# Optimization experiments

Hardware: AMD Instinct MI355X
Metric: run time of the kernel (lower is better)

## Reference

```python
import jax, jax.numpy as jnp
import numpy as np

# dims
N, E, B, T = 1024, 8192, 4, 8          # nodes, edges, batch, time steps
IN, HID, H, NCLASS = 64, 64, 4, 7      # in_dim, nhidden, heads, nclass
K = N - NCLASS + 1                     # output-head conv width
NEG, EPS = 0.2, 1e-5


def setup_inputs() -> dict:
    key = jax.random.key(0)
    ks = jax.random.split(key, 24)
    p = lambda i, shape: jax.random.normal(ks[i], shape, jnp.float32) * 0.05
    inputs = jax.random.normal(ks[0], (B, IN, T, N), jnp.float32)
    src = jax.random.randint(ks[1], (E,), 0, N, jnp.int32)
    dst = jnp.repeat(jnp.arange(N, dtype=jnp.int32), E // N)  # every node has in-degree 8
    return {
        "inputs": inputs, "src": src, "dst": dst,
        "W0": p(2, (H * HID, IN)), "al0": p(3, (H, HID)), "ar0": p(4, (H, HID)),
        "W1": p(5, (H * HID, H * HID)), "al1": p(6, (H, HID)), "ar1": p(7, (H, HID)),
        "W2": p(8, (H * 1, H * HID)), "al2": p(9, (H, 1)), "ar2": p(10, (H, 1)),
        "Wres2": p(11, (H * 1, H * HID)),
        # Outputlayer
        "tc1_w": p(12, (H, H, T)), "tc1_b": p(13, (H,)),
        "ln1_g": jnp.ones((N, H), jnp.float32), "ln1_b": jnp.zeros((N, H), jnp.float32),
        "tc2_w": p(14, (1, H)), "tc2_b": p(15, (1,)),
        "ln2_g": jnp.ones((N, 1), jnp.float32), "ln2_b": jnp.zeros((N, 1), jnp.float32),
        "fc_w": p(16, (K,)), "fc_b": p(17, (1,)),
    }


def _gat_conv(h, src, dst, W, al, ar, res=None, act=None):
    # h: (N,B,T,F) -> feat: (N,B,T,H,D)
    heads, d = al.shape
    feat = (h @ W.T).reshape(N, B, T, heads, d)
    el = jnp.einsum('nbthd,hd->nbth', feat, al)
    er = jnp.einsum('nbthd,hd->nbth', feat, ar)
    e = jax.nn.leaky_relu(el[src] + er[dst], NEG)           # (E,B,T,H)
    emax = jax.ops.segment_max(e, dst, num_segments=N)
    ex = jnp.exp(e - emax[dst])
    den = jax.ops.segment_sum(ex, dst, num_segments=N)
    a = ex / den[dst]                                        # edge softmax over incoming edges
    out = jax.ops.segment_sum(feat[src] * a[..., None], dst, num_segments=N)  # (N,B,T,H,D)
    if res is not None:
        out = out + res
    if act is not None:
        out = act(out)
    return out


def reference(inputs, src, dst,
              W0, al0, ar0, W1, al1, ar1, W2, al2, ar2, Wres2,
              tc1_w, tc1_b, ln1_g, ln1_b, tc2_w, tc2_b, ln2_g, ln2_b, fc_w, fc_b):
    # (B,IN,T,N) -> (N,B,T,IN) : transpose(0,3).transpose(1,3)
    h = jnp.transpose(inputs.astype(jnp.float32), (3, 0, 2, 1))
    h1 = _gat_conv(h, src, dst, W0, al0, ar0, act=jax.nn.elu).reshape(N, B, T, H * HID)
    h2 = _gat_conv(h1, src, dst, W1, al1, ar1,
                   res=h1.reshape(N, B, T, H, HID), act=jax.nn.elu).reshape(N, B, T, H * HID)
    res2 = (h2 @ Wres2.T).reshape(N, B, T, H, 1)
    o = _gat_conv(h2, src, dst, W2, al2, ar2, res=res2)      # (N,B,T,H,1)
    # transpose(1,3).transpose(0,3).squeeze(-1) -> (B,H,T,N)
    x = jnp.transpose(o[..., 0], (1, 3, 2, 0))

    # Outputlayer
    # tconv1: Conv2d(H->H, kernel (T,1)) collapses time -> (B,H,N)
    x1 = jnp.einsum('oht,bhtn->bon', tc1_w, x) + tc1_b[None, :, None]
    # ln1: LayerNorm over (N,H) of (B,1,N,H)
    z = jnp.transpose(x1, (0, 2, 1))                          # (B,N,H)
    mu = z.mean(axis=(1, 2), keepdims=True)
    var = z.var(axis=(1, 2), keepdims=True)
    z = (z - mu) / jnp.sqrt(var + EPS) * ln1_g + ln1_b
    x1 = jnp.transpose(z, (0, 2, 1))                          # (B,H,N)
    # tconv2: 1x1 conv H->1 -> (B,1,N)
    x2 = jnp.einsum('oh,bhn->bon', tc2_w, x1) + tc2_b[None, :, None]
    # ln2: LayerNorm over (N,1)
    mu = x2.mean(axis=2, keepdims=True)
    var = x2.var(axis=2, keepdims=True)
    x2 = (x2 - mu) / jnp.sqrt(var + EPS) * ln2_g[:, 0] + ln2_b[:, 0]
    # fc: Conv2d(1->1, kernel (1,K)) sliding over nodes -> (B,NCLASS)
    xc = x2[:, :, None, :]                                    # (B,1,1,N) NCHW
    w = fc_w[None, None, None, :]                             # (1,1,1,K) OIHW
    out = jax.lax.conv_general_dilated(xc, w, (1, 1), 'VALID') + fc_b[None, :, None, None]
    return out[:, 0, 0, :]                                    # (B, NCLASS)
```

## Files before the change

### kernel.cpp

```cpp
#include <hip/hip_runtime.h>
#include <math.h>

#define NEGS 0.2f
#define EPSF 1e-5f

typedef short s16x8 __attribute__((ext_vector_type(8)));
typedef float f32x4 __attribute__((ext_vector_type(4)));

__device__ __forceinline__ float b2f(unsigned short u) {
  union { unsigned int i; float f; } v; v.i = ((unsigned int)u) << 16; return v.f;
}
__device__ __forceinline__ unsigned short f2b(float f) {
  union { float f; unsigned int i; } v; v.f = f;
  unsigned int x = v.i;
  return (unsigned short)((x + 0x7fffu + ((x >> 16) & 1u)) >> 16);
}

__device__ __forceinline__ float block_reduce256(float v, float* red) {
  #pragma unroll
  for (int o = 32; o > 0; o >>= 1) v += __shfl_down(v, o);
  __syncthreads();
  if ((threadIdx.x & 63) == 0) red[threadIdx.x >> 6] = v;
  __syncthreads();
  return red[0] + red[1] + red[2] + red[3];
}

__global__ __launch_bounds__(256) void k_cvt(
    const float* __restrict__ inp, const float* __restrict__ W0,
    const float* __restrict__ W1, unsigned short* __restrict__ Xb,
    unsigned short* __restrict__ W0b, unsigned short* __restrict__ W1b)
{
  __shared__ float L[64][65];
  const int tid = threadIdx.x;
  if (blockIdx.x >= 512) {
    const int j = (blockIdx.x - 512) * 256 + tid;
    W0b[j] = f2b(W0[j]);
    float4 w4 = *(const float4*)&W1[j*4];
    ushort4 o4; o4.x = f2b(w4.x); o4.y = f2b(w4.y); o4.z = f2b(w4.z); o4.w = f2b(w4.w);
    *(ushort4*)&W1b[j*4] = o4;
    return;
  }
  const int blk = blockIdx.x;
  const int n0 = (blk & 15) * 64;
  const int t  = (blk >> 4) & 7;
  const int b  = blk >> 7;
  const int nn = tid & 63, ch0 = tid >> 6;
  #pragma unroll
  for (int ch = ch0; ch < 64; ch += 4)
    L[ch][nn] = inp[((size_t)(b*64 + ch)*8 + t)*1024 + n0 + nn];
  __syncthreads();
  const int r = tid >> 2, ck = tid & 3;
  s16x8 o0, o1;
  #pragma unroll
  for (int i = 0; i < 8; ++i) o0[i] = (short)f2b(L[ck*16 + i][r]);
  #pragma unroll
  for (int i = 0; i < 8; ++i) o1[i] = (short)f2b(L[ck*16 + 8 + i][r]);
  const int row = (n0 + r)*32 + b*8 + t;
  *(s16x8*)&Xb[(size_t)row*64 + ck*16]     = o0;
  *(s16x8*)&Xb[(size_t)row*64 + ck*16 + 8] = o1;
}

template<int KD>
__global__ __launch_bounds__(256) void k_feat_mfma(
    const unsigned short* __restrict__ X, const unsigned short* __restrict__ Wb,
    const float* __restrict__ al, const float* __restrict__ ar,
    unsigned short* __restrict__ feat, float* __restrict__ el, float* __restrict__ er)
{
  __shared__ __align__(16) unsigned short Lb[64*256];
  const int tid  = threadIdx.x;
  const int w    = tid >> 6;
  const int lane = tid & 63;
  const int n16  = lane & 15;
  const int q    = lane >> 4;
  const int r0   = blockIdx.x * 64;

  f32x4 acc[4][4];
  #pragma unroll
  for (int rt = 0; rt < 4; ++rt)
    #pragma unroll
    for (int ct = 0; ct < 4; ++ct) acc[rt][ct] = (f32x4){0.f,0.f,0.f,0.f};

  #pragma unroll
  for (int kc = 0; kc < KD/32; ++kc) {
    s16x8 af[4], bf[4];
    #pragma unroll
    for (int rt = 0; rt < 4; ++rt)
      af[rt] = *(const s16x8*)&X[(size_t)(r0 + rt*16 + n16)*KD + kc*32 + q*8];
    #pragma unroll
    for (int ct = 0; ct < 4; ++ct)
      bf[ct] = *(const s16x8*)&Wb[(size_t)((w*4 + ct)*16 + n16)*KD + kc*32 + q*8];
    #pragma unroll
    for (int rt = 0; rt < 4; ++rt)
      #pragma unroll
      for (int ct = 0; ct < 4; ++ct)
        acc[rt][ct] = __builtin_amdgcn_mfma_f32_16x16x32_bf16(af[rt], bf[ct], acc[rt][ct], 0, 0, 0);
  }

  float alv[4], arv[4];
  #pragma unroll
  for (int ct = 0; ct < 4; ++ct) {
    alv[ct] = al[w*64 + ct*16 + n16];
    arv[ct] = ar[w*64 + ct*16 + n16];
  }
  #pragma unroll
  for (int rt = 0; rt < 4; ++rt) {
    #pragma unroll
    for (int reg = 0; reg < 4; ++reg) {
      float pl = acc[rt][0][reg]*alv[0] + acc[rt][1][reg]*alv[1]
               + acc[rt][2][reg]*alv[2] + acc[rt][3][reg]*alv[3];
      float pr = acc[rt][0][reg]*arv[0] + acc[rt][1][reg]*arv[1]
               + acc[rt][2][reg]*arv[2] + acc[rt][3][reg]*arv[3];
      #pragma unroll
      for (int o = 1; o < 16; o <<= 1) { pl += __shfl_xor(pl, o); pr += __shfl_xor(pr, o); }
      if (n16 == 0) {
        int r = r0 + rt*16 + q*4 + reg;
        el[r*4 + w] = pl;
        er[r*4 + w] = pr;
      }
    }
  }

  #pragma unroll
  for (int rt = 0; rt < 4; ++rt)
    #pragma unroll
    for (int ct = 0; ct < 4; ++ct)
      #pragma unroll
      for (int reg = 0; reg < 4; ++reg)
        Lb[(rt*16 + q*4 + reg)*256 + w*64 + ct*16 + n16] = f2b(acc[rt][ct][reg]);
  __syncthreads();
  #pragma unroll
  for (int i = 0; i < 8; ++i) {
    int u = tid + i*256;
    int row = u >> 5, off = (u & 31) * 8;
    *(s16x8*)&feat[(size_t)(r0 + row)*256 + off] = *(const s16x8*)&Lb[row*256 + off];
  }
}

template<int RES, int STOREOUT, int PROJ>
__global__ __launch_bounds__(256) void k_agg(
    const unsigned short* __restrict__ feat, const float* __restrict__ el,
    const float* __restrict__ er, const int* __restrict__ src,
    const unsigned short* __restrict__ resin, unsigned short* __restrict__ out,
    const float* __restrict__ W2, const float* __restrict__ Wres2,
    float* __restrict__ feat2, float* __restrict__ res2)
{
  __shared__ float wsm[8][4][8][4];
  __shared__ int   ssm[8];
  __shared__ __align__(16) float Wp[8][256];
  const int n   = blockIdx.x;
  const int tid = threadIdx.x;
  if (tid < 8) ssm[tid] = src[n*8 + tid];
  if (PROJ) {
    for (int j = tid; j < 2048; j += 256) {
      int o = j >> 8, k = j & 255;
      Wp[o][k] = (o < 4) ? W2[o*256 + k] : Wres2[(o-4)*256 + k];
    }
  }
  __syncthreads();
  if (tid < 128) {
    const int h = tid & 3, t = (tid >> 2) & 7, b = tid >> 5;
    const int rn = n*32 + b*8 + t;
    const float erv = er[rn*4 + h];
    float e[8]; float m = -1e30f;
    #pragma unroll
    for (int j = 0; j < 8; ++j) {
      float v = el[(ssm[j]*32 + b*8 + t)*4 + h] + erv;
      v = v >= 0.f ? v : NEGS * v;
      e[j] = v; m = fmaxf(m, v);
    }
    float den = 0.f;
    #pragma unroll
    for (int j = 0; j < 8; ++j) { e[j] = __expf(e[j] - m); den += e[j]; }
    const float inv = 1.f / den;
    #pragma unroll
    for (int j = 0; j < 8; ++j) wsm[j][b][t][h] = e[j] * inv;
  }
  __syncthreads();
  const int b    = tid >> 6;
  const int lane = tid & 63;
  const int c0   = lane * 4;
  const int h    = lane >> 4;
  int s[8];
  #pragma unroll
  for (int j = 0; j < 8; ++j) s[j] = ssm[j];
  #pragma unroll 1
  for (int t = 0; t < 8; ++t) {
    const int rn = n*32 + b*8 + t;
    float a0=0.f, a1=0.f, a2=0.f, a3=0.f;
    #pragma unroll
    for (int j = 0; j < 8; ++j) {
      ushort4 u = *(const ushort4*)&feat[(size_t)(s[j]*32 + b*8 + t)*256 + c0];
      const float wj = wsm[j][b][t][h];
      a0 = fmaf(wj, b2f(u.x), a0); a1 = fmaf(wj, b2f(u.y), a1);
      a2 = fmaf(wj, b2f(u.z), a2); a3 = fmaf(wj, b2f(u.w), a3);
    }
    if (RES) {
      ushort4 rr = *(const ushort4*)&resin[(size_t)rn*256 + c0];
      a0 += b2f(rr.x); a1 += b2f(rr.y); a2 += b2f(rr.z); a3 += b2f(rr.w);
      a0 = a0 > 0.f ? a0 : expm1f(a0);
      a1 = a1 > 0.f ? a1 : expm1f(a1);
      a2 = a2 > 0.f ? a2 : expm1f(a2);
      a3 = a3 > 0.f ? a3 : expm1f(a3);
    } else {
      a0 = a0 > 0.f ? a0 : expm1f(a0);
      a1 = a1 > 0.f ? a1 : expm1f(a1);
      a2 = a2 > 0.f ? a2 : expm1f(a2);
      a3 = a3 > 0.f ? a3 : expm1f(a3);
    }
    if (STOREOUT) {
      ushort4 o;
      o.x = f2b(a0); o.y = f2b(a1); o.z = f2b(a2); o.w = f2b(a3);
      *(ushort4*)&out[(size_t)rn*256 + c0] = o;
    }
    if (PROJ) {
      #pragma unroll
      for (int o = 0; o < 8; ++o) {
        float4 w4 = *(const float4*)&Wp[o][c0];
        float p = a0*w4.x + a1*w4.y + a2*w4.z + a3*w4.w;
        #pragma unroll
        for (int off = 1; off < 64; off <<= 1) p += __shfl_xor(p, off);
        if (lane == 0) {
          if (o < 4) feat2[rn*4 + o] = p;
          else       res2[rn*4 + (o-4)] = p;
        }
      }
    }
  }
}

__global__ __launch_bounds__(128) void k_agg2(
    const float* __restrict__ feat2, const float* __restrict__ res2,
    const int* __restrict__ src, const float* __restrict__ al2,
    const float* __restrict__ ar2, const float* __restrict__ tc1w,
    const float* __restrict__ tc1b, float* __restrict__ x1)
{
  __shared__ float os[4][8][4];
  const int n = blockIdx.x;
  const int tid = threadIdx.x;
  const int b = tid >> 5, t = (tid >> 2) & 7, h = tid & 3;
  const int rn = n*32 + b*8 + t;
  const float av = al2[h], rv = ar2[h];
  const float erv = feat2[rn*4 + h] * rv;
  float f[8], e[8]; float m = -1e30f;
  #pragma unroll
  for (int j = 0; j < 8; ++j) {
    int s_ = src[n*8 + j];
    f[j] = feat2[(s_*32 + b*8 + t)*4 + h];
    float v = f[j]*av + erv;
    v = v >= 0.f ? v : NEGS * v;
    e[j] = v; m = fmaxf(m, v);
  }
  float den = 0.f, num = 0.f;
  #pragma unroll
  for (int j = 0; j < 8; ++j) { float ex = __expf(e[j]-m); den += ex; num = fmaf(ex, f[j], num); }
  os[b][t][h] = num/den + res2[rn*4 + h];
  __syncthreads();
  if (tid < 16) {
    int b2 = tid >> 2, o2 = tid & 3;
    float acc = tc1b[o2];
    #pragma unroll
    for (int hh = 0; hh < 4; ++hh)
      #pragma unroll
      for (int tt = 0; tt < 8; ++tt)
        acc = fmaf(tc1w[(o2*4 + hh)*8 + tt], os[b2][tt][hh], acc);
    x1[(b2*4 + o2)*1024 + n] = acc;
  }
}

__global__ __launch_bounds__(256) void k_final(
    const float* __restrict__ x1, const float* __restrict__ ln1g,
    const float* __restrict__ ln1b, const float* __restrict__ tc2w,
    const float* __restrict__ tc2b, const float* __restrict__ ln2g,
    const float* __restrict__ ln2b, const float* __restrict__ fcw,
    const float* __restrict__ fcb, float* __restrict__ out)
{
  __shared__ float red[4];
  __shared__ float x2s[1024];
  const int b = blockIdx.x;
  const int tid = threadIdx.x;
  float s = 0.f, q = 0.f;
  for (int j = tid; j < 4096; j += 256) {
    float v = x1[b*4096 + j];
    s += v; q += v*v;
  }
  float S = block_reduce256(s, red);
  float Q = block_reduce256(q, red);
  float mu  = S * (1.f/4096.f);
  float var = Q * (1.f/4096.f) - mu*mu;
  float inv = rsqrtf(var + EPSF);
  float tb = tc2b[0];
  float s2 = 0.f, q2 = 0.f;
  for (int nn = tid; nn < 1024; nn += 256) {
    float acc = tb;
    #pragma unroll
    for (int h = 0; h < 4; ++h) {
      float z = (x1[b*4096 + h*1024 + nn] - mu) * inv * ln1g[nn*4 + h] + ln1b[nn*4 + h];
      acc = fmaf(tc2w[h], z, acc);
    }
    x2s[nn] = acc;
    s2 += acc; q2 += acc*acc;
  }
  float S2 = block_reduce256(s2, red);
  float Q2 = block_reduce256(q2, red);
  float mu2  = S2 * (1.f/1024.f);
  float inv2 = rsqrtf(Q2 * (1.f/1024.f) - mu2*mu2 + EPSF);
  __syncthreads();
  for (int nn = tid; nn < 1024; nn += 256)
    x2s[nn] = (x2s[nn] - mu2) * inv2 * ln2g[nn] + ln2b[nn];
  __syncthreads();
  for (int c = 0; c < 7; ++c) {
    float p = 0.f;
    for (int k = tid; k < 1018; k += 256) p = fmaf(x2s[c + k], fcw[k], p);
    float P = block_reduce256(p, red);
    if (tid == 0) out[b*7 + c] = P + fcb[0];
  }
}

extern "C" void kernel_launch(void* const* d_in, const int* in_sizes, int n_in,
                              void* d_out, int out_size, void* d_ws, size_t ws_size,
                              hipStream_t stream)
{
  const float* inp  = (const float*)d_in[0];
  const int*   src  = (const int*)  d_in[1];
  const float* W0   = (const float*)d_in[3];
  const float* al0  = (const float*)d_in[4];
  const float* ar0  = (const float*)d_in[5];
  const float* W1   = (const float*)d_in[6];
  const float* al1  = (const float*)d_in[7];
  const float* ar1  = (const float*)d_in[8];
  const float* W2   = (const float*)d_in[9];
  const float* al2  = (const float*)d_in[10];
  const float* ar2  = (const float*)d_in[11];
  const float* Wr2  = (const float*)d_in[12];
  const float* tc1w = (const float*)d_in[13];
  const float* tc1b = (const float*)d_in[14];
  const float* ln1g = (const float*)d_in[15];
  const float* ln1b = (const float*)d_in[16];
  const float* tc2w = (const float*)d_in[17];
  const float* tc2b = (const float*)d_in[18];
  const float* ln2g = (const float*)d_in[19];
  const float* ln2b = (const float*)d_in[20];
  const float* fcw  = (const float*)d_in[21];
  const float* fcb  = (const float*)d_in[22];
  float* out = (float*)d_out;

  unsigned short* Xb    = (unsigned short*)d_ws;
  unsigned short* W0b   = Xb    + 2097152;
  unsigned short* W1b   = W0b   + 16384;
  unsigned short* featb = W1b   + 65536;
  unsigned short* h1b   = featb + 8388608;
  float* el    = (float*)(h1b + 8388608);
  float* er    = el    + 131072;
  float* feat2 = er    + 131072;
  float* res2  = feat2 + 131072;
  float* x1    = res2  + 131072;

  k_cvt<<<dim3(576), dim3(256), 0, stream>>>(inp, W0, W1, Xb, W0b, W1b);
  k_feat_mfma<64><<<dim3(512), dim3(256), 0, stream>>>(Xb, W0b, al0, ar0, featb, el, er);
  k_agg<0,1,0><<<dim3(1024), dim3(256), 0, stream>>>(featb, el, er, src,
      (const unsigned short*)nullptr, h1b, nullptr, nullptr, nullptr, nullptr);
  k_feat_mfma<256><<<dim3(512), dim3(256), 0, stream>>>(h1b, W1b, al1, ar1, featb, el, er);
  k_agg<1,0,1><<<dim3(1024), dim3(256), 0, stream>>>(featb, el, er, src,
      h1b, (unsigned short*)nullptr, W2, Wr2, feat2, res2);
  k_agg2<<<dim3(1024), dim3(128), 0, stream>>>(feat2, res2, src, al2, ar2, tc1w, tc1b, x1);
  k_final<<<dim3(4), dim3(256), 0, stream>>>(x1, ln1g, ln1b, tc2w, tc2b, ln2g, ln2b, fcw, fcb, out);
}
```

Baseline: 202.7 us.

## Fuse layer-0 aggregation with layer-1 MFMA projection and widen aggregation loads

Layer-0 edge-softmax aggregation is merged into the layer-1 feature-projection kernel. Each block handles two nodes (64 rows), writes the aggregated rows into LDS and feeds them straight into the bf16 MFMA GEMM, which removes one launch and the global read-back of h1b. Feature buffers are double-buffered (featb0/featb1, el0/el1) because the fused kernel reads layer-0 features while writing layer-1 ones. The layer-1 aggregation kernel also moves to two nodes per block with 8-wide bf16 loads. The trade-off is more LDS per block and each block re-reading W1 from global memory.

```diff
diff --git a/kernel.cpp b/kernel.cpp
--- a/kernel.cpp
+++ b/kernel.cpp
@@ -136,35 +136,160 @@
   }
 }
 
-template<int RES, int STOREOUT, int PROJ>
-__global__ __launch_bounds__(256) void k_agg(
-    const unsigned short* __restrict__ feat, const float* __restrict__ el,
+__global__ __launch_bounds__(256) void k_agg0_feat1(
+    const unsigned short* __restrict__ feat0, const float* __restrict__ el0,
+    const float* __restrict__ er0, const int* __restrict__ src,
+    const unsigned short* __restrict__ W1b, const float* __restrict__ al,
+    const float* __restrict__ ar, unsigned short* __restrict__ h1b,
+    unsigned short* __restrict__ feat1, float* __restrict__ el1, float* __restrict__ er1)
+{
+  __shared__ float wsm[2][8][4][8][4];
+  __shared__ int   ssm[2][8];
+  __shared__ __align__(16) unsigned short smbuf[64*264];
+  unsigned short (*At)[264] = (unsigned short(*)[264])smbuf;
+  unsigned short *Lb = smbuf;
+  const int tid = threadIdx.x;
+  const int n0  = blockIdx.x * 2;
+  if (tid < 16) ssm[tid>>3][tid&7] = src[(n0 + (tid>>3))*8 + (tid&7)];
+  __syncthreads();
+  {
+    const int u = tid >> 7, b = (tid >> 5) & 3, t = (tid >> 2) & 7, h = tid & 3;
+    const int rn = (n0 + u)*32 + b*8 + t;
+    const float erv = er0[rn*4 + h];
+    float e[8]; float m = -1e30f;
+    #pragma unroll
+    for (int j = 0; j < 8; ++j) {
+      float v = el0[(ssm[u][j]*32 + b*8 + t)*4 + h] + erv;
+      v = v >= 0.f ? v : NEGS * v;
+      e[j] = v; m = fmaxf(m, v);
+    }
+    float den = 0.f;
+    #pragma unroll
+    for (int j = 0; j < 8; ++j) { e[j] = __expf(e[j] - m); den += e[j]; }
+    const float inv = 1.f / den;
+    #pragma unroll
+    for (int j = 0; j < 8; ++j) wsm[u][j][b][t][h] = e[j] * inv;
+  }
+  __syncthreads();
+  {
+    const int hw2 = tid >> 5;
+    const int l5  = tid & 31;
+    const int c0  = l5 * 8;
+    const int hh  = l5 >> 3;
+    #pragma unroll 1
+    for (int pass = 0; pass < 8; ++pass) {
+      const int row = pass*8 + hw2;
+      const int u = row >> 5, bb = (row >> 3) & 3, tt = row & 7;
+      float a[8] = {0.f,0.f,0.f,0.f,0.f,0.f,0.f,0.f};
+      #pragma unroll
+      for (int j = 0; j < 8; ++j) {
+        const int rs = ssm[u][j]*32 + bb*8 + tt;
+        s16x8 v = *(const s16x8*)&feat0[(size_t)rs*256 + c0];
+        const float wj = wsm[u][j][bb][tt][hh];
+        #pragma unroll
+        for (int i = 0; i < 8; ++i) a[i] = fmaf(wj, b2f((unsigned short)v[i]), a[i]);
+      }
+      s16x8 o;
+      #pragma unroll
+      for (int i = 0; i < 8; ++i) {
+        float x = a[i] > 0.f ? a[i] : expm1f(a[i]);
+        o[i] = (short)f2b(x);
+      }
+      *(s16x8*)&At[row][c0] = o;
+      *(s16x8*)&h1b[(size_t)(n0*32 + row)*256 + c0] = o;
+    }
+  }
+  __syncthreads();
+  const int w    = tid >> 6;
+  const int lane = tid & 63;
+  const int n16  = lane & 15;
+  const int q    = lane >> 4;
+  const int r0   = n0 * 32;
+  f32x4 acc[4][4];
+  #pragma unroll
+  for (int rt = 0; rt < 4; ++rt)
+    #pragma unroll
+    for (int ct = 0; ct < 4; ++ct) acc[rt][ct] = (f32x4){0.f,0.f,0.f,0.f};
+  #pragma unroll
+  for (int kc = 0; kc < 8; ++kc) {
+    s16x8 af[4], bf[4];
+    #pragma unroll
+    for (int rt = 0; rt < 4; ++rt)
+      af[rt] = *(const s16x8*)&At[rt*16 + n16][kc*32 + q*8];
+    #pragma unroll
+    for (int ct = 0; ct < 4; ++ct)
+      bf[ct] = *(const s16x8*)&W1b[(size_t)((w*4 + ct)*16 + n16)*256 + kc*32 + q*8];
+    #pragma unroll
+    for (int rt = 0; rt < 4; ++rt)
+      #pragma unroll
+      for (int ct = 0; ct < 4; ++ct)
+        acc[rt][ct] = __builtin_amdgcn_mfma_f32_16x16x32_bf16(af[rt], bf[ct], acc[rt][ct], 0, 0, 0);
+  }
+  float alv[4], arv[4];
+  #pragma unroll
+  for (int ct = 0; ct < 4; ++ct) {
+    alv[ct] = al[w*64 + ct*16 + n16];
+    arv[ct] = ar[w*64 + ct*16 + n16];
+  }
+  #pragma unroll
+  for (int rt = 0; rt < 4; ++rt) {
+    #pragma unroll
+    for (int reg = 0; reg < 4; ++reg) {
+      float pl = acc[rt][0][reg]*alv[0] + acc[rt][1][reg]*alv[1]
+               + acc[rt][2][reg]*alv[2] + acc[rt][3][reg]*alv[3];
+      float pr = acc[rt][0][reg]*arv[0] + acc[rt][1][reg]*arv[1]
+               + acc[rt][2][reg]*arv[2] + acc[rt][3][reg]*arv[3];
+      #pragma unroll
+      for (int o = 1; o < 16; o <<= 1) { pl += __shfl_xor(pl, o); pr += __shfl_xor(pr, o); }
+      if (n16 == 0) {
+        int r = r0 + rt*16 + q*4 + reg;
+        el1[r*4 + w] = pl;
+        er1[r*4 + w] = pr;
+      }
+    }
+  }
+  __syncthreads();
+  #pragma unroll
+  for (int rt = 0; rt < 4; ++rt)
+    #pragma unroll
+    for (int ct = 0; ct < 4; ++ct)
+      #pragma unroll
+      for (int reg = 0; reg < 4; ++reg)
+        Lb[(rt*16 + q*4 + reg)*256 + w*64 + ct*16 + n16] = f2b(acc[rt][ct][reg]);
+  __syncthreads();
+  #pragma unroll
+  for (int i = 0; i < 8; ++i) {
+    int u = tid + i*256;
+    int row = u >> 5, off = (u & 31) * 8;
+    *(s16x8*)&feat1[(size_t)(r0 + row)*256 + off] = *(const s16x8*)&Lb[row*256 + off];
+  }
+}
+
+__global__ __launch_bounds__(256) void k_agg1_proj(
+    const unsigned short* __restrict__ feat1, const float* __restrict__ el,
     const float* __restrict__ er, const int* __restrict__ src,
-    const unsigned short* __restrict__ resin, unsigned short* __restrict__ out,
-    const float* __restrict__ W2, const float* __restrict__ Wres2,
-    float* __restrict__ feat2, float* __restrict__ res2)
-{
-  __shared__ float wsm[8][4][8][4];
-  __shared__ int   ssm[8];
+    const unsigned short* __restrict__ h1b, const float* __restrict__ W2,
+    const float* __restrict__ Wres2, float* __restrict__ feat2, float* __restrict__ res2)
+{
+  __shared__ float wsm[2][8][4][8][4];
+  __shared__ int   ssm[2][8];
   __shared__ __align__(16) float Wp[8][256];
-  const int n   = blockIdx.x;
   const int tid = threadIdx.x;
-  if (tid < 8) ssm[tid] = src[n*8 + tid];
-  if (PROJ) {
-    for (int j = tid; j < 2048; j += 256) {
-      int o = j >> 8, k = j & 255;
-      Wp[o][k] = (o < 4) ? W2[o*256 + k] : Wres2[(o-4)*256 + k];
-    }
-  }
-  __syncthreads();
-  if (tid < 128) {
-    const int h = tid & 3, t = (tid >> 2) & 7, b = tid >> 5;
-    const int rn = n*32 + b*8 + t;
+  const int n0  = blockIdx.x * 2;
+  if (tid < 16) ssm[tid>>3][tid&7] = src[(n0 + (tid>>3))*8 + (tid&7)];
+  for (int j2 = tid; j2 < 2048; j2 += 256) {
+    int o = j2 >> 8, k = j2 & 255;
+    Wp[o][k] = (o < 4) ? W2[o*256 + k] : Wres2[(o-4)*256 + k];
+  }
+  __syncthreads();
+  {
+    const int u = tid >> 7, b = (tid >> 5) & 3, t = (tid >> 2) & 7, h = tid & 3;
+    const int rn = (n0 + u)*32 + b*8 + t;
     const float erv = er[rn*4 + h];
     float e[8]; float m = -1e30f;
     #pragma unroll
     for (int j = 0; j < 8; ++j) {
-      float v = el[(ssm[j]*32 + b*8 + t)*4 + h] + erv;
+      float v = el[(ssm[u][j]*32 + b*8 + t)*4 + h] + erv;
       v = v >= 0.f ? v : NEGS * v;
       e[j] = v; m = fmaxf(m, v);
     }
@@ -173,56 +298,44 @@
     for (int j = 0; j < 8; ++j) { e[j] = __expf(e[j] - m); den += e[j]; }
     const float inv = 1.f / den;
     #pragma unroll
-    for (int j = 0; j < 8; ++j) wsm[j][b][t][h] = e[j] * inv;
-  }
-  __syncthreads();
-  const int b    = tid >> 6;
-  const int lane = tid & 63;
-  const int c0   = lane * 4;
-  const int h    = lane >> 4;
-  int s[8];
-  #pragma unroll
-  for (int j = 0; j < 8; ++j) s[j] = ssm[j];
+    for (int j = 0; j < 8; ++j) wsm[u][j][b][t][h] = e[j] * inv;
+  }
+  __syncthreads();
+  const int b  = tid >> 6;
+  const int hw = (tid >> 5) & 1;
+  const int l5 = tid & 31;
+  const int c0 = l5 * 8;
+  const int hh = l5 >> 3;
   #pragma unroll 1
-  for (int t = 0; t < 8; ++t) {
-    const int rn = n*32 + b*8 + t;
-    float a0=0.f, a1=0.f, a2=0.f, a3=0.f;
+  for (int ut = 0; ut < 8; ++ut) {
+    const int u = ut >> 2, t = (ut & 3)*2 + hw;
+    const int rn = (n0 + u)*32 + b*8 + t;
+    float a[8] = {0.f,0.f,0.f,0.f,0.f,0.f,0.f,0.f};
     #pragma unroll
     for (int j = 0; j < 8; ++j) {
-      ushort4 u = *(const ushort4*)&feat[(size_t)(s[j]*32 + b*8 + t)*256 + c0];
-      const float wj = wsm[j][b][t][h];
-      a0 = fmaf(wj, b2f(u.x), a0); a1 = fmaf(wj, b2f(u.y), a1);
-      a2 = fmaf(wj, b2f(u.z), a2); a3 = fmaf(wj, b2f(u.w), a3);
-    }
-    if (RES) {
-      ushort4 rr = *(const ushort4*)&resin[(size_t)rn*256 + c0];
-      a0 += b2f(rr.x); a1 += b2f(rr.y); a2 += b2f(rr.z); a3 += b2f(rr.w);
-      a0 = a0 > 0.f ? a0 : expm1f(a0);
-      a1 = a1 > 0.f ? a1 : expm1f(a1);
-      a2 = a2 > 0.f ? a2 : expm1f(a2);
-      a3 = a3 > 0.f ? a3 : expm1f(a3);
-    } else {
-      a0 = a0 > 0.f ? a0 : expm1f(a0);
-      a1 = a1 > 0.f ? a1 : expm1f(a1);
-      a2 = a2 > 0.f ? a2 : expm1f(a2);
-      a3 = a3 > 0.f ? a3 : expm1f(a3);
-    }
-    if (STOREOUT) {
-      ushort4 o;
-      o.x = f2b(a0); o.y = f2b(a1); o.z = f2b(a2); o.w = f2b(a3);
-      *(ushort4*)&out[(size_t)rn*256 + c0] = o;
-    }
-    if (PROJ) {
-      #pragma unroll
-      for (int o = 0; o < 8; ++o) {
-        float4 w4 = *(const float4*)&Wp[o][c0];
-        float p = a0*w4.x + a1*w4.y + a2*w4.z + a3*w4.w;
-        #pragma unroll
-        for (int off = 1; off < 64; off <<= 1) p += __shfl_xor(p, off);
-        if (lane == 0) {
-          if (o < 4) feat2[rn*4 + o] = p;
-          else       res2[rn*4 + (o-4)] = p;
-        }
+      const int rs = ssm[u][j]*32 + b*8 + t;
+      s16x8 v = *(const s16x8*)&feat1[(size_t)rs*256 + c0];
+      const float wj = wsm[u][j][b][t][hh];
+      #pragma unroll
+      for (int i = 0; i < 8; ++i) a[i] = fmaf(wj, b2f((unsigned short)v[i]), a[i]);
+    }
+    s16x8 rr = *(const s16x8*)&h1b[(size_t)rn*256 + c0];
+    #pragma unroll
+    for (int i = 0; i < 8; ++i) {
+      float x = a[i] + b2f((unsigned short)rr[i]);
+      a[i] = x > 0.f ? x : expm1f(x);
+    }
+    #pragma unroll
+    for (int o = 0; o < 8; ++o) {
+      float4 wa = *(const float4*)&Wp[o][c0];
+      float4 wb = *(const float4*)&Wp[o][c0 + 4];
+      float p = a[0]*wa.x + a[1]*wa.y + a[2]*wa.z + a[3]*wa.w
+              + a[4]*wb.x + a[5]*wb.y + a[6]*wb.z + a[7]*wb.w;
+      #pragma unroll
+      for (int off = 1; off < 32; off <<= 1) p += __shfl_xor(p, off);
+      if (l5 == 0) {
+        if (o < 4) feat2[rn*4 + o] = p;
+        else       res2[rn*4 + (o-4)] = p;
       }
     }
   }
@@ -344,24 +457,26 @@
   const float* fcb  = (const float*)d_in[22];
   float* out = (float*)d_out;
 
-  unsigned short* Xb    = (unsigned short*)d_ws;
-  unsigned short* W0b   = Xb    + 2097152;
-  unsigned short* W1b   = W0b   + 16384;
-  unsigned short* featb = W1b   + 65536;
-  unsigned short* h1b   = featb + 8388608;
-  float* el    = (float*)(h1b + 8388608);
-  float* er    = el    + 131072;
-  float* feat2 = er    + 131072;
+  unsigned short* Xb     = (unsigned short*)d_ws;
+  unsigned short* W0b    = Xb     + 2097152;
+  unsigned short* W1b    = W0b    + 16384;
+  unsigned short* featb0 = W1b    + 65536;
+  unsigned short* featb1 = featb0 + 8388608;
+  unsigned short* h1b    = featb1 + 8388608;
+  float* el0   = (float*)(h1b + 8388608);
+  float* er0   = el0   + 131072;
+  float* el1   = er0   + 131072;
+  float* er1   = el1   + 131072;
+  float* feat2 = er1   + 131072;
   float* res2  = feat2 + 131072;
   float* x1    = res2  + 131072;
 
   k_cvt<<<dim3(576), dim3(256), 0, stream>>>(inp, W0, W1, Xb, W0b, W1b);
-  k_feat_mfma<64><<<dim3(512), dim3(256), 0, stream>>>(Xb, W0b, al0, ar0, featb, el, er);
-  k_agg<0,1,0><<<dim3(1024), dim3(256), 0, stream>>>(featb, el, er, src,
-      (const unsigned short*)nullptr, h1b, nullptr, nullptr, nullptr, nullptr);
-  k_feat_mfma<256><<<dim3(512), dim3(256), 0, stream>>>(h1b, W1b, al1, ar1, featb, el, er);
-  k_agg<1,0,1><<<dim3(1024), dim3(256), 0, stream>>>(featb, el, er, src,
-      h1b, (unsigned short*)nullptr, W2, Wr2, feat2, res2);
+  k_feat_mfma<64><<<dim3(512), dim3(256), 0, stream>>>(Xb, W0b, al0, ar0, featb0, el0, er0);
+  k_agg0_feat1<<<dim3(512), dim3(256), 0, stream>>>(featb0, el0, er0, src, W1b, al1, ar1,
+                                                    h1b, featb1, el1, er1);
+  k_agg1_proj<<<dim3(512), dim3(256), 0, stream>>>(featb1, el1, er1, src, h1b, W2, Wr2,
+                                                   feat2, res2);
   k_agg2<<<dim3(1024), dim3(128), 0, stream>>>(feat2, res2, src, al2, ar2, tc1w, tc1b, x1);
   k_final<<<dim3(4), dim3(256), 0, stream>>>(x1, ln1g, ln1b, tc2w, tc2b, ln2g, ln2b, fcw, fcb, out);
 }
```

Measured after the change: 208.0 us. 2.6% more time.
